# Performance work log

Measured on AMD Instinct MI355X. Metric: run time of the kernel, lower is better.

The kernel has to match this reference:

```python
import jax, jax.numpy as jnp
import numpy as np

NUM_NODES = 100000
NUM_EDGES = 1600000
NUM_GRAPHS = 512
HIDDEN = 128
LAYERS = 3
NUM_CLASSES = 10
BN_EPS = 1e-5


def setup_inputs() -> dict:
    key = jax.random.key(0)
    ks = jax.random.split(key, 12)
    x = jax.random.normal(ks[0], (NUM_NODES, HIDDEN), dtype=jnp.float32)
    edge_index = jax.random.randint(ks[1], (2, NUM_EDGES), 0, NUM_NODES, dtype=jnp.int32)
    batch = jnp.sort(jax.random.randint(ks[2], (NUM_NODES,), 0, NUM_GRAPHS, dtype=jnp.int32))
    s = 1.0 / np.sqrt(HIDDEN)
    W1 = jax.random.normal(ks[3], (LAYERS, HIDDEN, HIDDEN), dtype=jnp.float32) * s
    b1 = jnp.zeros((LAYERS, HIDDEN), dtype=jnp.float32)
    W2 = jax.random.normal(ks[4], (LAYERS, HIDDEN, HIDDEN), dtype=jnp.float32) * s
    b2 = jnp.zeros((LAYERS, HIDDEN), dtype=jnp.float32)
    gamma = jnp.ones((LAYERS, HIDDEN), dtype=jnp.float32)
    beta = jnp.zeros((LAYERS, HIDDEN), dtype=jnp.float32)
    eps_gin = jnp.zeros((LAYERS,), dtype=jnp.float32)  # train_eps init 0
    lin1_w = jax.random.normal(ks[5], (LAYERS * HIDDEN, HIDDEN), dtype=jnp.float32) * (1.0 / np.sqrt(LAYERS * HIDDEN))
    lin1_b = jnp.zeros((HIDDEN,), dtype=jnp.float32)
    lin2_w = jax.random.normal(ks[6], (HIDDEN, NUM_CLASSES), dtype=jnp.float32) * s
    lin2_b = jnp.zeros((NUM_CLASSES,), dtype=jnp.float32)
    return {"x": x, "edge_index": edge_index, "batch": batch,
            "W1": W1, "b1": b1, "W2": W2, "b2": b2,
            "gamma": gamma, "beta": beta, "eps_gin": eps_gin,
            "lin1_w": lin1_w, "lin1_b": lin1_b, "lin2_w": lin2_w, "lin2_b": lin2_b}


def _batchnorm(h, g, b):
    mu = jnp.mean(h, axis=0, keepdims=True)
    var = jnp.var(h, axis=0, keepdims=True)
    return (h - mu) * jax.lax.rsqrt(var + BN_EPS) * g + b


def reference(x, edge_index, batch, W1, b1, W2, b2, gamma, beta, eps_gin,
              lin1_w, lin1_b, lin2_w, lin2_b):
    src, dst = edge_index[0], edge_index[1]
    n = x.shape[0]
    h = x
    layer_hs = []
    for l in range(LAYERS):
        # scatter-add neighbor aggregation: agg[i] = sum_{j->i} h[j]
        agg = jax.ops.segment_sum(h[src], dst, num_segments=n)
        z = (1.0 + eps_gin[l]) * h + agg
        z = jax.nn.relu(z @ W1[l] + b1[l])
        z = jax.nn.relu(z @ W2[l] + b2[l])
        h = _batchnorm(z, gamma[l], beta[l])
        layer_hs.append(h)
    h_cat = jnp.concatenate(layer_hs, axis=-1)  # [N, LAYERS*HIDDEN]
    # global mean pool per graph
    sums = jax.ops.segment_sum(h_cat, batch, num_segments=NUM_GRAPHS)
    counts = jax.ops.segment_sum(jnp.ones((n, 1), h_cat.dtype), batch, num_segments=NUM_GRAPHS)
    g = sums / jnp.maximum(counts, 1.0)
    g = jax.nn.relu(g @ lin1_w + lin1_b)
    # dropout is identity in inference
    return g @ lin2_w + lin2_b
```

## Files before the change

### kernel.cpp

```cpp
#include <hip/hip_runtime.h>

#define HID 128
#define NGRAPH 512
#define NLAYERS 3
#define BN_EPS 1e-5f
#define NPB 256
#define EB 4096

typedef __attribute__((ext_vector_type(8))) short bf16x8;
typedef __attribute__((ext_vector_type(4))) float f32x4;
typedef __attribute__((ext_vector_type(2))) float f32x2;

__device__ inline unsigned short f2bf(float x) {
    union { float f; unsigned u; } v; v.f = x;
    unsigned r = v.u + 0x7FFFu + ((v.u >> 16) & 1u);
    return (unsigned short)(r >> 16);
}
__device__ inline float bf2f(unsigned short b) {
    union { float f; unsigned u; } v; v.u = ((unsigned)b) << 16; return v.f;
}
__device__ inline f32x2 bfp(unsigned u) {
    union { unsigned q; float f; } lo, hi;
    lo.q = u << 16; hi.q = u & 0xFFFF0000u;
    f32x2 r; r[0] = lo.f; r[1] = hi.f; return r;
}

__global__ void k_prep(float* __restrict__ stats, float* __restrict__ gsum,
                       const float4* __restrict__ x4, ushort* __restrict__ xb, int total4,
                       const float* __restrict__ W1, ushort* __restrict__ w1h, ushort* __restrict__ w1l,
                       const float* __restrict__ W2, ushort* __restrict__ w2h, ushort* __restrict__ w2l,
                       int wtotal, int xblocks,
                       const int* __restrict__ dst, int E, int* __restrict__ blkcnt) {
    __shared__ int hist[512];
    int b = blockIdx.x, t = threadIdx.x;
    if (b < 768) {
        if (b == 0) for (int l = 0; l < NLAYERS; ++l) stats[l * 256 + t] = 0.0f;
        gsum[b * 256 + t] = 0.0f;
    } else if (b < 1152) {
        int gid = (b - 768) * 256 + t;
        const float* W; ushort *Wh, *Wl; int e;
        if (gid < wtotal) { W = W1; Wh = w1h; Wl = w1l; e = gid; }
        else              { W = W2; Wh = w2h; Wl = w2l; e = gid - wtotal; }
        if (e < wtotal) {
            int l = e >> 14, rem = e & 16383, k = rem >> 7, n = rem & 127;
            float v = W[e];
            ushort hi = f2bf(v);
            ushort lo = f2bf(v - bf2f(hi));
            int o = (l << 14) + (n << 7) + k;
            Wh[o] = hi; Wl[o] = lo;
        }
    } else if (b < 1152 + xblocks) {
        int i = (b - 1152) * 256 + t;
        if (i < total4) {
            float4 v = x4[i];
            uint2 p;
            p.x = ((unsigned)f2bf(v.y) << 16) | f2bf(v.x);
            p.y = ((unsigned)f2bf(v.w) << 16) | f2bf(v.z);
            ((uint2*)xb)[i] = p;
        }
    } else {
        int b2 = b - (1152 + xblocks);
        hist[t] = 0; hist[t + 256] = 0;
        __syncthreads();
        int base = b2 * EB;
        #pragma unroll
        for (int i = 0; i < 16; ++i) {
            int e = base + i * 256 + t;
            if (e < E) atomicAdd(&hist[dst[e] >> 8], 1);
        }
        __syncthreads();
        blkcnt[b2 * 512 + t]       = hist[t];
        blkcnt[b2 * 512 + t + 256] = hist[t + 256];
    }
}

__global__ __launch_bounds__(256) void k_btot_reduce(const int* __restrict__ blkcnt,
                                                     int eblk, int* __restrict__ tot) {
    __shared__ int sh[256];
    int b = blockIdx.x;
    int t = threadIdx.x;
    int s = 0;
    for (int j = t; j < eblk; j += 256) s += blkcnt[j * 512 + b];
    sh[t] = s;
    __syncthreads();
    #pragma unroll
    for (int k = 128; k > 0; k >>= 1) {
        if (t < k) sh[t] += sh[t + k];
        __syncthreads();
    }
    if (t == 0) tot[b] = sh[0];
}

__global__ __launch_bounds__(512) void k_bscan(const int* __restrict__ tot, int nb, int E,
                                               int* __restrict__ bbase, int* __restrict__ rowptrN) {
    __shared__ int sh[512];
    int t = threadIdx.x;
    sh[t] = (t < nb) ? tot[t] : 0;
    __syncthreads();
    #pragma unroll
    for (int s = 1; s < 512; s <<= 1) {
        int v = (t >= s) ? sh[t - s] : 0;
        __syncthreads();
        sh[t] += v;
        __syncthreads();
    }
    if (t < nb) bbase[t] = (t == 0) ? 0 : sh[t - 1];
    if (t == 0) { bbase[nb] = E; *rowptrN = E; }
}

__global__ __launch_bounds__(512) void k_colscan(int* __restrict__ blkcnt, int eblk,
                                                 const int* __restrict__ bbase) {
    __shared__ int sh[512];
    int t = threadIdx.x;
    int b = blockIdx.x;
    sh[t] = (t < eblk) ? blkcnt[t * 512 + b] : 0;
    __syncthreads();
    #pragma unroll
    for (int s = 1; s < 512; s <<= 1) {
        int v = (t >= s) ? sh[t - s] : 0;
        __syncthreads();
        sh[t] += v;
        __syncthreads();
    }
    int excl = (t == 0) ? 0 : sh[t - 1];
    if (t < eblk) blkcnt[t * 512 + b] = bbase[b] + excl;
}

__global__ __launch_bounds__(256) void k_bscatter(const int* __restrict__ src,
                                                  const int* __restrict__ dst, int E,
                                                  const int* __restrict__ blkcnt,
                                                  unsigned* __restrict__ pairs) {
    __shared__ int hist[512];
    __shared__ int lbase[512];
    int t = threadIdx.x;
    hist[t] = 0; hist[t + 256] = 0;
    lbase[t]       = blkcnt[blockIdx.x * 512 + t];
    lbase[t + 256] = blkcnt[blockIdx.x * 512 + t + 256];
    __syncthreads();
    int base = blockIdx.x * EB;
    #pragma unroll
    for (int i = 0; i < 16; ++i) {
        int e = base + i * 256 + t;
        if (e < E) {
            int d = dst[e];
            int b = d >> 8;
            int pos = lbase[b] + atomicAdd(&hist[b], 1);
            pairs[pos] = ((unsigned)(d & 255) << 24) | (unsigned)src[e];
        }
    }
}

__global__ __launch_bounds__(256) void k_bbuild(const unsigned* __restrict__ pairs,
                                                const int* __restrict__ bbase, int N,
                                                int* __restrict__ rowptr, int* __restrict__ csr) {
    __shared__ int cnt[256];
    __shared__ int off[256];
    int t = threadIdx.x;
    int b = blockIdx.x;
    int base = bbase[b], bcount = bbase[b + 1] - base;
    cnt[t] = 0;
    __syncthreads();
    for (int i = t; i < bcount; i += 256) atomicAdd(&cnt[pairs[base + i] >> 24], 1);
    __syncthreads();
    off[t] = cnt[t];
    __syncthreads();
    for (int s = 1; s < 256; s <<= 1) {
        int v = (t >= s) ? off[t - s] : 0;
        __syncthreads();
        off[t] += v;
        __syncthreads();
    }
    int excl = (t == 0) ? 0 : off[t - 1];
    int node = b * NPB + t;
    if (node < N) rowptr[node] = base + excl;
    cnt[t] = excl;
    __syncthreads();
    for (int i = t; i < bcount; i += 256) {
        unsigned p = pairs[base + i];
        int dl = p >> 24;
        int pos = base + atomicAdd(&cnt[dl], 1);
        csr[pos] = (int)(p & 0xFFFFFFu);
    }
}

__global__ __launch_bounds__(256, 4) void k_gin_layer(
        const int* __restrict__ rowptr, const int* __restrict__ csr_src,
        const uint2* __restrict__ hinb,
        const float* __restrict__ prev_stats,
        const float* __restrict__ g_row, const float* __restrict__ be_row,
        const float* __restrict__ eps_gin, int layer, const int* __restrict__ batch,
        const ushort* __restrict__ w1h, const ushort* __restrict__ w1l,
        const float* __restrict__ b1,
        const ushort* __restrict__ w2h, const ushort* __restrict__ w2l,
        const float* __restrict__ b2,
        ushort* __restrict__ Hout, float* __restrict__ stat_sum, float* __restrict__ stat_sq,
        float* __restrict__ gsum, int N) {
    __shared__ __align__(16) ushort smem[8192];

    const int t = threadIdx.x;
    const int lane = t & 63;
    const int wv = t >> 6;
    const int li = lane & 15;
    const int kq = lane >> 4;
    const int n0 = wv * 32;
    const int row0 = blockIdx.x * 64;
    const int swz = (li & 7) * 4;

    {
        int q = lane >> 4;
        int f = lane & 15;
        f32x2 scv2[4], shv2[4];
        if (prev_stats) {
            float invn = 1.0f / (float)N;
            #pragma unroll
            for (int d = 0; d < 4; ++d) {
                #pragma unroll
                for (int h = 0; h < 2; ++h) {
                    int fi = f * 8 + d * 2 + h;
                    float mu = prev_stats[fi] * invn;
                    float var = prev_stats[128 + fi] * invn - mu * mu;
                    float inv = rsqrtf(var + BN_EPS);
                    float scj = g_row[fi] * inv;
                    scv2[d][h] = scj; shv2[d][h] = be_row[fi] - mu * scj;
                }
            }
        } else {
            #pragma unroll
            for (int d = 0; d < 4; ++d) { scv2[d] = (f32x2){1.f, 1.f}; shv2[d] = (f32x2){0.f, 0.f}; }
        }
        float e1 = 1.0f + eps_gin[layer];
        const uint4* hin4 = (const uint4*)hinb;
        #pragma unroll
        for (int it = 0; it < 4; ++it) {
            int r = wv * 16 + it * 4 + q;
            int node = row0 + r;
            f32x2 a2[4];
            #pragma unroll
            for (int d = 0; d < 4; ++d) a2[d] = (f32x2){0.f, 0.f};
            float cdeg = 0.f;
            if (node < N) {
                int beg = rowptr[node], end = rowptr[node + 1];
                uint4 hv = hin4[(size_t)node * 16 + f];
                a2[0] = e1 * bfp(hv.x); a2[1] = e1 * bfp(hv.y);
                a2[2] = e1 * bfp(hv.z); a2[3] = e1 * bfp(hv.w);
                int p = beg;
                for (; p + 8 <= end; p += 8) {
                    int s0 = csr_src[p],     s1 = csr_src[p + 1], s2 = csr_src[p + 2], s3 = csr_src[p + 3];
                    int s4 = csr_src[p + 4], s5 = csr_src[p + 5], s6 = csr_src[p + 6], s7 = csr_src[p + 7];
                    uint4 v0 = hin4[(size_t)s0 * 16 + f];
                    uint4 v1 = hin4[(size_t)s1 * 16 + f];
                    uint4 v2 = hin4[(size_t)s2 * 16 + f];
                    uint4 v3 = hin4[(size_t)s3 * 16 + f];
                    uint4 v4 = hin4[(size_t)s4 * 16 + f];
                    uint4 v5 = hin4[(size_t)s5 * 16 + f];
                    uint4 v6 = hin4[(size_t)s6 * 16 + f];
                    uint4 v7 = hin4[(size_t)s7 * 16 + f];
                    a2[0] += ((bfp(v0.x) + bfp(v1.x)) + (bfp(v2.x) + bfp(v3.x)))
                           + ((bfp(v4.x) + bfp(v5.x)) + (bfp(v6.x) + bfp(v7.x)));
                    a2[1] += ((bfp(v0.y) + bfp(v1.y)) + (bfp(v2.y) + bfp(v3.y)))
                           + ((bfp(v4.y) + bfp(v5.y)) + (bfp(v6.y) + bfp(v7.y)));
                    a2[2] += ((bfp(v0.z) + bfp(v1.z)) + (bfp(v2.z) + bfp(v3.z)))
                           + ((bfp(v4.z) + bfp(v5.z)) + (bfp(v6.z) + bfp(v7.z)));
                    a2[3] += ((bfp(v0.w) + bfp(v1.w)) + (bfp(v2.w) + bfp(v3.w)))
                           + ((bfp(v4.w) + bfp(v5.w)) + (bfp(v6.w) + bfp(v7.w)));
                }
                if (p < end) {
                    int last = end - 1;
                    int c1 = min(p + 1, last), c2 = min(p + 2, last), c3 = min(p + 3, last);
                    int c4 = min(p + 4, last), c5 = min(p + 5, last), c6 = min(p + 6, last);
                    int c7 = min(p + 7, last);
                    int s0 = csr_src[p],  s1 = csr_src[c1], s2 = csr_src[c2], s3 = csr_src[c3];
                    int s4 = csr_src[c4], s5 = csr_src[c5], s6 = csr_src[c6], s7 = csr_src[c7];
                    uint4 v0 = hin4[(size_t)s0 * 16 + f];
                    uint4 v1 = hin4[(size_t)s1 * 16 + f];
                    uint4 v2 = hin4[(size_t)s2 * 16 + f];
                    uint4 v3 = hin4[(size_t)s3 * 16 + f];
                    uint4 v4 = hin4[(size_t)s4 * 16 + f];
                    uint4 v5 = hin4[(size_t)s5 * 16 + f];
                    uint4 v6 = hin4[(size_t)s6 * 16 + f];
                    uint4 v7 = hin4[(size_t)s7 * 16 + f];
                    int rem = end - p;
                    unsigned m1 = (rem > 1) ? 0xFFFFFFFFu : 0u;
                    unsigned m2 = (rem > 2) ? 0xFFFFFFFFu : 0u;
                    unsigned m3 = (rem > 3) ? 0xFFFFFFFFu : 0u;
                    unsigned m4 = (rem > 4) ? 0xFFFFFFFFu : 0u;
                    unsigned m5 = (rem > 5) ? 0xFFFFFFFFu : 0u;
                    unsigned m6 = (rem > 6) ? 0xFFFFFFFFu : 0u;
                    a2[0] += ((bfp(v0.x) + bfp(v1.x & m1)) + (bfp(v2.x & m2) + bfp(v3.x & m3)))
                           + ((bfp(v4.x & m4) + bfp(v5.x & m5)) + (bfp(v6.x & m6) + (f32x2){0.f, 0.f}));
                    a2[1] += ((bfp(v0.y) + bfp(v1.y & m1)) + (bfp(v2.y & m2) + bfp(v3.y & m3)))
                           + ((bfp(v4.y & m4) + bfp(v5.y & m5)) + (bfp(v6.y & m6) + (f32x2){0.f, 0.f}));
                    a2[2] += ((bfp(v0.z) + bfp(v1.z & m1)) + (bfp(v2.z & m2) + bfp(v3.z & m3)))
                           + ((bfp(v4.z & m4) + bfp(v5.z & m5)) + (bfp(v6.z & m6) + (f32x2){0.f, 0.f}));
                    a2[3] += ((bfp(v0.w) + bfp(v1.w & m1)) + (bfp(v2.w & m2) + bfp(v3.w & m3)))
                           + ((bfp(v4.w & m4) + bfp(v5.w & m5)) + (bfp(v6.w & m6) + (f32x2){0.f, 0.f}));
                    (void)v7;
                }
                cdeg = e1 + (float)(end - beg);
            }
            f32x2 rr2[4];
            #pragma unroll
            for (int d = 0; d < 4; ++d) rr2[d] = scv2[d] * a2[d] + cdeg * shv2[d];
            uint4 ph;
            ph.x = ((unsigned)f2bf(rr2[0][1]) << 16) | f2bf(rr2[0][0]);
            ph.y = ((unsigned)f2bf(rr2[1][1]) << 16) | f2bf(rr2[1][0]);
            ph.z = ((unsigned)f2bf(rr2[2][1]) << 16) | f2bf(rr2[2][0]);
            ph.w = ((unsigned)f2bf(rr2[3][1]) << 16) | f2bf(rr2[3][0]);
            int d = r * 16 + (f ^ (r & 7));
            ((uint4*)smem)[d] = ph;
        }
    }
    __syncthreads();

    f32x4 acc[4][2];
    #pragma unroll
    for (int i = 0; i < 4; ++i) {
        acc[i][0] = (f32x4){0.f, 0.f, 0.f, 0.f};
        acc[i][1] = (f32x4){0.f, 0.f, 0.f, 0.f};
    }

    #pragma unroll
    for (int ch = 0; ch < 2; ++ch) {
        #pragma unroll
        for (int ks = 0; ks < 2; ++ks) {
            int kcol = ch * 8 + ks * 4 + kq;
            bf16x8 bh[2], bl[2];
            #pragma unroll
            for (int nt = 0; nt < 2; ++nt) {
                size_t wo = (size_t)(n0 + nt * 16 + li) * 128 + (ch * 64 + ks * 32 + kq * 8);
                bh[nt] = *(const bf16x8*)&w1h[wo];
                bl[nt] = *(const bf16x8*)&w1l[wo];
            }
            #pragma unroll
            for (int mt = 0; mt < 4; ++mt) {
                int r = mt * 16 + li;
                int hw = (r * 16 + (kcol ^ (li & 7))) * 8;
                bf16x8 ah = *(const bf16x8*)&smem[hw];
                #pragma unroll
                for (int nt = 0; nt < 2; ++nt) {
                    acc[mt][nt] = __builtin_amdgcn_mfma_f32_16x16x32_bf16(ah, bh[nt], acc[mt][nt], 0, 0, 0);
                    acc[mt][nt] = __builtin_amdgcn_mfma_f32_16x16x32_bf16(ah, bl[nt], acc[mt][nt], 0, 0, 0);
                }
            }
        }
    }

    float bz0 = b1[n0 + li], bz1 = b1[n0 + 16 + li];
    __syncthreads();
    #pragma unroll
    for (int mt = 0; mt < 4; ++mt) {
        #pragma unroll
        for (int nt = 0; nt < 2; ++nt) {
            int c = n0 + nt * 16 + li;
            int dk = c >> 1;
            int halfbase = (dk >> 5) * 32;
            int dlow = dk & 31;
            int codd = c & 1;
            float bias = nt ? bz1 : bz0;
            #pragma unroll
            for (int reg = 0; reg < 4; ++reg) {
                int r = mt * 16 + kq * 4 + reg;
                float v = fmaxf(acc[mt][nt][reg] + bias, 0.f);
                int us = (r * 64 + halfbase + (dlow ^ ((r & 7) * 4))) * 2 + codd;
                smem[us] = f2bf(v);
            }
        }
    }
    #pragma unroll
    for (int i = 0; i < 4; ++i) {
        acc[i][0] = (f32x4){0.f, 0.f, 0.f, 0.f};
        acc[i][1] = (f32x4){0.f, 0.f, 0.f, 0.f};
    }
    __syncthreads();

    #pragma unroll
    for (int ch = 0; ch < 2; ++ch) {
        #pragma unroll
        for (int ks = 0; ks < 2; ++ks) {
            bf16x8 bh[2], bl[2];
            #pragma unroll
            for (int nt = 0; nt < 2; ++nt) {
                size_t wo = (size_t)(n0 + nt * 16 + li) * 128 + (ch * 64 + ks * 32 + kq * 8);
                bh[nt] = *(const bf16x8*)&w2h[wo];
                bl[nt] = *(const bf16x8*)&w2l[wo];
            }
            int aoff = (ks * 16 + kq * 4) ^ swz;
            #pragma unroll
            for (int mt = 0; mt < 4; ++mt) {
                int idx = ((mt * 16 + li) * 64 + ch * 32 + aoff) * 2;
                bf16x8 ah = *(const bf16x8*)&smem[idx];
                #pragma unroll
                for (int nt = 0; nt < 2; ++nt) {
                    acc[mt][nt] = __builtin_amdgcn_mfma_f32_16x16x32_bf16(ah, bh[nt], acc[mt][nt], 0, 0, 0);
                    acc[mt][nt] = __builtin_amdgcn_mfma_f32_16x16x32_bf16(ah, bl[nt], acc[mt][nt], 0, 0, 0);
                }
            }
        }
    }

    float bb0 = b2[n0 + li], bb1 = b2[n0 + 16 + li];
    int btr[4][4];
    #pragma unroll
    for (int mt = 0; mt < 4; ++mt)
        #pragma unroll
        for (int reg = 0; reg < 4; ++reg) {
            int grow = row0 + mt * 16 + kq * 4 + reg;
            btr[mt][reg] = (grow < N) ? batch[grow] : -1;
        }
    __syncthreads();
    float s0 = 0.f, q0 = 0.f, s1 = 0.f, q1 = 0.f;
    #pragma unroll
    for (int mt = 0; mt < 4; ++mt) {
        #pragma unroll
        for (int reg = 0; reg < 4; ++reg) {
            int r = mt * 16 + kq * 4 + reg;
            float v0 = fmaxf(acc[mt][0][reg] + bb0, 0.f);
            float v1 = fmaxf(acc[mt][1][reg] + bb1, 0.f);
            smem[r * 128 + n0 + li]      = f2bf(v0);
            smem[r * 128 + n0 + 16 + li] = f2bf(v1);
            if (btr[mt][reg] >= 0) {
                s0 += v0; q0 += v0 * v0; s1 += v1; q1 += v1 * v1;
            }
        }
    }
    __syncthreads();
    {
        int valid = N - row0; if (valid > 64) valid = 64;
        int tot = valid * 16;
        for (int i = t; i < tot; i += 256) {
            int r = i >> 4, c = i & 15;
            ((uint4*)&Hout[(size_t)(row0 + r) * HID])[c] = ((const uint4*)smem)[r * 16 + c];
        }
    }
    s0 += __shfl_xor(s0, 16); s0 += __shfl_xor(s0, 32);
    q0 += __shfl_xor(q0, 16); q0 += __shfl_xor(q0, 32);
    s1 += __shfl_xor(s1, 16); s1 += __shfl_xor(s1, 32);
    q1 += __shfl_xor(q1, 16); q1 += __shfl_xor(q1, 32);
    if (kq == 0) {
        unsafeAtomicAdd(&stat_sum[n0 + li], s0);
        unsafeAtomicAdd(&stat_sq[n0 + li], q0);
        unsafeAtomicAdd(&stat_sum[n0 + 16 + li], s1);
        unsafeAtomicAdd(&stat_sq[n0 + 16 + li], q1);
    }
    int lastr = N - 1; if (lastr > row0 + 63) lastr = row0 + 63;
    int g_lo = batch[row0], g_hi = batch[lastr];
    int loff = layer * HID;
    for (int g = g_lo; g <= g_hi; ++g) {
        float p0 = 0.f, p1 = 0.f;
        #pragma unroll
        for (int mt = 0; mt < 4; ++mt)
            #pragma unroll
            for (int reg = 0; reg < 4; ++reg) {
                if (btr[mt][reg] == g) {
                    p0 += fmaxf(acc[mt][0][reg] + bb0, 0.f);
                    p1 += fmaxf(acc[mt][1][reg] + bb1, 0.f);
                }
            }
        p0 += __shfl_xor(p0, 16); p0 += __shfl_xor(p0, 32);
        p1 += __shfl_xor(p1, 16); p1 += __shfl_xor(p1, 32);
        if (kq == 0) {
            unsafeAtomicAdd(&gsum[(size_t)g * 384 + loff + n0 + li], p0);
            unsafeAtomicAdd(&gsum[(size_t)g * 384 + loff + n0 + 16 + li], p1);
        }
    }
}

__global__ __launch_bounds__(128) void k_mlp(const int* __restrict__ batch, int N,
                     const float* __restrict__ gsum, const float* __restrict__ stats,
                     const float* __restrict__ gamma, const float* __restrict__ beta,
                     const float* __restrict__ w1, const float* __restrict__ b1,
                     const float* __restrict__ w2, const float* __restrict__ b2,
                     float* __restrict__ out) {
    __shared__ float gl[384];
    __shared__ float hh[128];
    int g = blockIdx.x, t = threadIdx.x;
    int start, end;
    { int lo = 0, hi = N; while (lo < hi) { int m = (lo + hi) >> 1; if (batch[m] < g) lo = m + 1; else hi = m; } start = lo; }
    { int lo = start, hi = N; while (lo < hi) { int m = (lo + hi) >> 1; if (batch[m] < g + 1) lo = m + 1; else hi = m; } end = lo; }
    float cnt = (float)(end - start);
    float invc = 1.0f / fmaxf(cnt, 1.0f);
    float invn = 1.0f / (float)N;
    #pragma unroll
    for (int l = 0; l < NLAYERS; ++l) {
        float mu = stats[l * 256 + t] * invn;
        float var = stats[l * 256 + 128 + t] * invn - mu * mu;
        float inv = rsqrtf(var + BN_EPS);
        float sc = gamma[l * HID + t] * inv;
        float sh = beta[l * HID + t] - mu * sc;
        gl[l * 128 + t] = (gsum[(size_t)g * 384 + l * 128 + t] * sc + sh * cnt) * invc;
    }
    __syncthreads();
    float acc = b1[t];
    for (int k = 0; k < 384; ++k) acc = fmaf(gl[k], w1[k * HID + t], acc);
    hh[t] = fmaxf(acc, 0.f);
    __syncthreads();
    if (t < 10) {
        float a2 = b2[t];
        for (int k = 0; k < 128; ++k) a2 = fmaf(hh[k], w2[k * 10 + t], a2);
        out[g * 10 + t] = a2;
    }
}

extern "C" void kernel_launch(void* const* d_in, const int* in_sizes, int n_in,
                              void* d_out, int out_size, void* d_ws, size_t ws_size,
                              hipStream_t stream) {
    const float* x     = (const float*)d_in[0];
    const int*   ei    = (const int*)d_in[1];
    const int*   batch = (const int*)d_in[2];
    const float* W1    = (const float*)d_in[3];
    const float* b1    = (const float*)d_in[4];
    const float* W2    = (const float*)d_in[5];
    const float* b2    = (const float*)d_in[6];
    const float* gamma = (const float*)d_in[7];
    const float* beta  = (const float*)d_in[8];
    const float* epsg  = (const float*)d_in[9];
    const float* l1w   = (const float*)d_in[10];
    const float* l1b   = (const float*)d_in[11];
    const float* l2w   = (const float*)d_in[12];
    const float* l2b   = (const float*)d_in[13];

    const int N = in_sizes[0] / HID;
    const int E = in_sizes[1] / 2;
    const int* src = ei;
    const int* dst = ei + E;
    const int nb = (N + NPB - 1) / NPB;
    const int eblk = (E + EB - 1) / EB;

    float* w = (float*)d_ws;
    const size_t NF = (size_t)N * HID;
    float* zbuf   = w;
    ushort* xb    = (ushort*)(w + NF);
    ushort* hb[3] = { xb + NF, xb + 2 * NF, xb + 3 * NF };
    float* stats  = w + 4 * NF;
    float* gsum   = stats + 768;
    int*   rowptr = (int*)(gsum + (size_t)NGRAPH * 384);
    int*   csr    = rowptr + N + 1;
    int*   bbase  = csr + E;
    int*   btot   = bbase + nb + 2;
    ushort* wt  = (ushort*)(((uintptr_t)(btot + nb + 1) + 15) & ~(uintptr_t)15);
    ushort* w1h = wt;
    ushort* w1l = wt + 49152;
    ushort* w2h = wt + 98304;
    ushort* w2l = wt + 147456;

    unsigned* pairs  = (unsigned*)zbuf;
    int*      blkcnt = (int*)(w + 2 * 1024 * 1024);

    const int total4 = (int)(NF / 4);
    const int xblocks = (total4 + 255) / 256;
    const int prep_blocks = 1152 + xblocks + eblk;
    k_prep<<<prep_blocks, 256, 0, stream>>>(stats, gsum, (const float4*)x, xb, total4,
                                            W1, w1h, w1l, W2, w2h, w2l, NLAYERS * HID * HID,
                                            xblocks, dst, E, blkcnt);

    k_btot_reduce<<<nb, 256, 0, stream>>>(blkcnt, eblk, btot);
    k_bscan<<<1, 512, 0, stream>>>(btot, nb, E, bbase, rowptr + N);
    k_colscan<<<nb, 512, 0, stream>>>(blkcnt, eblk, bbase);
    k_bscatter<<<eblk, 256, 0, stream>>>(src, dst, E, blkcnt, pairs);
    k_bbuild<<<nb, 256, 0, stream>>>(pairs, bbase, N, rowptr, csr);

    for (int l = 0; l < NLAYERS; ++l) {
        const ushort* hin = (l == 0) ? xb : hb[l - 1];
        const float* pstats = (l == 0) ? nullptr : (stats + (l - 1) * 256);
        const float* grow_  = gamma + (l == 0 ? 0 : (l - 1)) * HID;
        const float* brow_  = beta  + (l == 0 ? 0 : (l - 1)) * HID;

        k_gin_layer<<<(N + 63) / 64, 256, 0, stream>>>(
            rowptr, csr, (const uint2*)hin, pstats, grow_, brow_,
            epsg, l, batch,
            w1h + (size_t)l * 16384, w1l + (size_t)l * 16384, b1 + l * HID,
            w2h + (size_t)l * 16384, w2l + (size_t)l * 16384, b2 + l * HID,
            hb[l], stats + l * 256, stats + l * 256 + 128, gsum, N);
    }

    k_mlp<<<NGRAPH, 128, 0, stream>>>(batch, N, gsum, stats, gamma, beta,
                                      l1w, l1b, l2w, l2b, (float*)d_out);
}
```

Before: 504.2 us.

## Split fused GIN layer into separate aggregation and dense MLP kernels

The fused per-layer kernel is split in two. A new gather-aggregation kernel handles 16 nodes per block and runs at higher occupancy (launch bounds 6) with no shared memory. It applies the previous layer's batchnorm and writes the aggregated features as bf16 to a new global buffer. A separate dense kernel reloads that buffer into swizzled shared memory for the two MFMA matmuls. The aim is to hide the latency of the irregular gathers better by decoupling them from the register- and LDS-heavy GEMM. The cost is an extra global write and read of an N×128 bf16 tensor per layer plus an extra launch. The tail loop now also issues 7 gathers instead of 8.

```diff
diff --git a/kernel.cpp b/kernel.cpp
--- a/kernel.cpp
+++ b/kernel.cpp
@@ -183,12 +183,116 @@
     }
 }
 
-__global__ __launch_bounds__(256, 4) void k_gin_layer(
+__global__ __launch_bounds__(256, 6) void k_agg(
         const int* __restrict__ rowptr, const int* __restrict__ csr_src,
         const uint2* __restrict__ hinb,
         const float* __restrict__ prev_stats,
         const float* __restrict__ g_row, const float* __restrict__ be_row,
-        const float* __restrict__ eps_gin, int layer, const int* __restrict__ batch,
+        const float* __restrict__ eps_gin, int layer,
+        ushort* __restrict__ z0out, int N) {
+    const int t = threadIdx.x;
+    const int lane = t & 63;
+    const int wv = t >> 6;
+    const int q = lane >> 4;
+    const int f = lane & 15;
+
+    f32x2 scv2[4], shv2[4];
+    if (prev_stats) {
+        float invn = 1.0f / (float)N;
+        #pragma unroll
+        for (int d = 0; d < 4; ++d) {
+            #pragma unroll
+            for (int h = 0; h < 2; ++h) {
+                int fi = f * 8 + d * 2 + h;
+                float mu = prev_stats[fi] * invn;
+                float var = prev_stats[128 + fi] * invn - mu * mu;
+                float inv = rsqrtf(var + BN_EPS);
+                float scj = g_row[fi] * inv;
+                scv2[d][h] = scj; shv2[d][h] = be_row[fi] - mu * scj;
+            }
+        }
+    } else {
+        #pragma unroll
+        for (int d = 0; d < 4; ++d) { scv2[d] = (f32x2){1.f, 1.f}; shv2[d] = (f32x2){0.f, 0.f}; }
+    }
+    float e1 = 1.0f + eps_gin[layer];
+    const uint4* hin4 = (const uint4*)hinb;
+
+    int r = blockIdx.x * 16 + wv * 4 + q;
+    f32x2 a2[4];
+    #pragma unroll
+    for (int d = 0; d < 4; ++d) a2[d] = (f32x2){0.f, 0.f};
+    float cdeg = 0.f;
+    if (r < N) {
+        int beg = rowptr[r], end = rowptr[r + 1];
+        uint4 hv = hin4[(size_t)r * 16 + f];
+        a2[0] = e1 * bfp(hv.x); a2[1] = e1 * bfp(hv.y);
+        a2[2] = e1 * bfp(hv.z); a2[3] = e1 * bfp(hv.w);
+        int p = beg;
+        for (; p + 8 <= end; p += 8) {
+            int s0 = csr_src[p],     s1 = csr_src[p + 1], s2 = csr_src[p + 2], s3 = csr_src[p + 3];
+            int s4 = csr_src[p + 4], s5 = csr_src[p + 5], s6 = csr_src[p + 6], s7 = csr_src[p + 7];
+            uint4 v0 = hin4[(size_t)s0 * 16 + f];
+            uint4 v1 = hin4[(size_t)s1 * 16 + f];
+            uint4 v2 = hin4[(size_t)s2 * 16 + f];
+            uint4 v3 = hin4[(size_t)s3 * 16 + f];
+            uint4 v4 = hin4[(size_t)s4 * 16 + f];
+            uint4 v5 = hin4[(size_t)s5 * 16 + f];
+            uint4 v6 = hin4[(size_t)s6 * 16 + f];
+            uint4 v7 = hin4[(size_t)s7 * 16 + f];
+            a2[0] += ((bfp(v0.x) + bfp(v1.x)) + (bfp(v2.x) + bfp(v3.x)))
+                   + ((bfp(v4.x) + bfp(v5.x)) + (bfp(v6.x) + bfp(v7.x)));
+            a2[1] += ((bfp(v0.y) + bfp(v1.y)) + (bfp(v2.y) + bfp(v3.y)))
+                   + ((bfp(v4.y) + bfp(v5.y)) + (bfp(v6.y) + bfp(v7.y)));
+            a2[2] += ((bfp(v0.z) + bfp(v1.z)) + (bfp(v2.z) + bfp(v3.z)))
+                   + ((bfp(v4.z) + bfp(v5.z)) + (bfp(v6.z) + bfp(v7.z)));
+            a2[3] += ((bfp(v0.w) + bfp(v1.w)) + (bfp(v2.w) + bfp(v3.w)))
+                   + ((bfp(v4.w) + bfp(v5.w)) + (bfp(v6.w) + bfp(v7.w)));
+        }
+        if (p < end) {
+            int last = end - 1;
+            int c1 = min(p + 1, last), c2 = min(p + 2, last), c3 = min(p + 3, last);
+            int c4 = min(p + 4, last), c5 = min(p + 5, last), c6 = min(p + 6, last);
+            int s0 = csr_src[p],  s1 = csr_src[c1], s2 = csr_src[c2], s3 = csr_src[c3];
+            int s4 = csr_src[c4], s5 = csr_src[c5], s6 = csr_src[c6];
+            uint4 v0 = hin4[(size_t)s0 * 16 + f];
+            uint4 v1 = hin4[(size_t)s1 * 16 + f];
+            uint4 v2 = hin4[(size_t)s2 * 16 + f];
+            uint4 v3 = hin4[(size_t)s3 * 16 + f];
+            uint4 v4 = hin4[(size_t)s4 * 16 + f];
+            uint4 v5 = hin4[(size_t)s5 * 16 + f];
+            uint4 v6 = hin4[(size_t)s6 * 16 + f];
+            int rem = end - p;
+            unsigned m1 = (rem > 1) ? 0xFFFFFFFFu : 0u;
+            unsigned m2 = (rem > 2) ? 0xFFFFFFFFu : 0u;
+            unsigned m3 = (rem > 3) ? 0xFFFFFFFFu : 0u;
+            unsigned m4 = (rem > 4) ? 0xFFFFFFFFu : 0u;
+            unsigned m5 = (rem > 5) ? 0xFFFFFFFFu : 0u;
+            unsigned m6 = (rem > 6) ? 0xFFFFFFFFu : 0u;
+            a2[0] += ((bfp(v0.x) + bfp(v1.x & m1)) + (bfp(v2.x & m2) + bfp(v3.x & m3)))
+                   + ((bfp(v4.x & m4) + bfp(v5.x & m5)) + bfp(v6.x & m6));
+            a2[1] += ((bfp(v0.y) + bfp(v1.y & m1)) + (bfp(v2.y & m2) + bfp(v3.y & m3)))
+                   + ((bfp(v4.y & m4) + bfp(v5.y & m5)) + bfp(v6.y & m6));
+            a2[2] += ((bfp(v0.z) + bfp(v1.z & m1)) + (bfp(v2.z & m2) + bfp(v3.z & m3)))
+                   + ((bfp(v4.z & m4) + bfp(v5.z & m5)) + bfp(v6.z & m6));
+            a2[3] += ((bfp(v0.w) + bfp(v1.w & m1)) + (bfp(v2.w & m2) + bfp(v3.w & m3)))
+                   + ((bfp(v4.w & m4) + bfp(v5.w & m5)) + bfp(v6.w & m6));
+        }
+        cdeg = e1 + (float)(end - beg);
+    }
+    f32x2 rr2[4];
+    #pragma unroll
+    for (int d = 0; d < 4; ++d) rr2[d] = scv2[d] * a2[d] + cdeg * shv2[d];
+    uint4 ph;
+    ph.x = ((unsigned)f2bf(rr2[0][1]) << 16) | f2bf(rr2[0][0]);
+    ph.y = ((unsigned)f2bf(rr2[1][1]) << 16) | f2bf(rr2[1][0]);
+    ph.z = ((unsigned)f2bf(rr2[2][1]) << 16) | f2bf(rr2[2][0]);
+    ph.w = ((unsigned)f2bf(rr2[3][1]) << 16) | f2bf(rr2[3][0]);
+    if (r < N) ((uint4*)z0out)[(size_t)r * 16 + f] = ph;
+}
+
+__global__ __launch_bounds__(256, 4) void k_mlp_dense(
+        const uint4* __restrict__ z0, int layer, const int* __restrict__ batch,
         const ushort* __restrict__ w1h, const ushort* __restrict__ w1l,
         const float* __restrict__ b1,
         const ushort* __restrict__ w2h, const ushort* __restrict__ w2l,
@@ -196,7 +300,6 @@
         ushort* __restrict__ Hout, float* __restrict__ stat_sum, float* __restrict__ stat_sq,
         float* __restrict__ gsum, int N) {
     __shared__ __align__(16) ushort smem[8192];
-
     const int t = threadIdx.x;
     const int lane = t & 63;
     const int wv = t >> 6;
@@ -207,107 +310,13 @@
     const int swz = (li & 7) * 4;
 
     {
-        int q = lane >> 4;
-        int f = lane & 15;
-        f32x2 scv2[4], shv2[4];
-        if (prev_stats) {
-            float invn = 1.0f / (float)N;
-            #pragma unroll
-            for (int d = 0; d < 4; ++d) {
-                #pragma unroll
-                for (int h = 0; h < 2; ++h) {
-                    int fi = f * 8 + d * 2 + h;
-                    float mu = prev_stats[fi] * invn;
-                    float var = prev_stats[128 + fi] * invn - mu * mu;
-                    float inv = rsqrtf(var + BN_EPS);
-                    float scj = g_row[fi] * inv;
-                    scv2[d][h] = scj; shv2[d][h] = be_row[fi] - mu * scj;
-                }
-            }
-        } else {
-            #pragma unroll
-            for (int d = 0; d < 4; ++d) { scv2[d] = (f32x2){1.f, 1.f}; shv2[d] = (f32x2){0.f, 0.f}; }
-        }
-        float e1 = 1.0f + eps_gin[layer];
-        const uint4* hin4 = (const uint4*)hinb;
-        #pragma unroll
-        for (int it = 0; it < 4; ++it) {
-            int r = wv * 16 + it * 4 + q;
-            int node = row0 + r;
-            f32x2 a2[4];
-            #pragma unroll
-            for (int d = 0; d < 4; ++d) a2[d] = (f32x2){0.f, 0.f};
-            float cdeg = 0.f;
-            if (node < N) {
-                int beg = rowptr[node], end = rowptr[node + 1];
-                uint4 hv = hin4[(size_t)node * 16 + f];
-                a2[0] = e1 * bfp(hv.x); a2[1] = e1 * bfp(hv.y);
-                a2[2] = e1 * bfp(hv.z); a2[3] = e1 * bfp(hv.w);
-                int p = beg;
-                for (; p + 8 <= end; p += 8) {
-                    int s0 = csr_src[p],     s1 = csr_src[p + 1], s2 = csr_src[p + 2], s3 = csr_src[p + 3];
-                    int s4 = csr_src[p + 4], s5 = csr_src[p + 5], s6 = csr_src[p + 6], s7 = csr_src[p + 7];
-                    uint4 v0 = hin4[(size_t)s0 * 16 + f];
-                    uint4 v1 = hin4[(size_t)s1 * 16 + f];
-                    uint4 v2 = hin4[(size_t)s2 * 16 + f];
-                    uint4 v3 = hin4[(size_t)s3 * 16 + f];
-                    uint4 v4 = hin4[(size_t)s4 * 16 + f];
-                    uint4 v5 = hin4[(size_t)s5 * 16 + f];
-                    uint4 v6 = hin4[(size_t)s6 * 16 + f];
-                    uint4 v7 = hin4[(size_t)s7 * 16 + f];
-                    a2[0] += ((bfp(v0.x) + bfp(v1.x)) + (bfp(v2.x) + bfp(v3.x)))
-                           + ((bfp(v4.x) + bfp(v5.x)) + (bfp(v6.x) + bfp(v7.x)));
-                    a2[1] += ((bfp(v0.y) + bfp(v1.y)) + (bfp(v2.y) + bfp(v3.y)))
-                           + ((bfp(v4.y) + bfp(v5.y)) + (bfp(v6.y) + bfp(v7.y)));
-                    a2[2] += ((bfp(v0.z) + bfp(v1.z)) + (bfp(v2.z) + bfp(v3.z)))
-                           + ((bfp(v4.z) + bfp(v5.z)) + (bfp(v6.z) + bfp(v7.z)));
-                    a2[3] += ((bfp(v0.w) + bfp(v1.w)) + (bfp(v2.w) + bfp(v3.w)))
-                           + ((bfp(v4.w) + bfp(v5.w)) + (bfp(v6.w) + bfp(v7.w)));
-                }
-                if (p < end) {
-                    int last = end - 1;
-                    int c1 = min(p + 1, last), c2 = min(p + 2, last), c3 = min(p + 3, last);
-                    int c4 = min(p + 4, last), c5 = min(p + 5, last), c6 = min(p + 6, last);
-                    int c7 = min(p + 7, last);
-                    int s0 = csr_src[p],  s1 = csr_src[c1], s2 = csr_src[c2], s3 = csr_src[c3];
-                    int s4 = csr_src[c4], s5 = csr_src[c5], s6 = csr_src[c6], s7 = csr_src[c7];
-                    uint4 v0 = hin4[(size_t)s0 * 16 + f];
-                    uint4 v1 = hin4[(size_t)s1 * 16 + f];
-                    uint4 v2 = hin4[(size_t)s2 * 16 + f];
-                    uint4 v3 = hin4[(size_t)s3 * 16 + f];
-                    uint4 v4 = hin4[(size_t)s4 * 16 + f];
-                    uint4 v5 = hin4[(size_t)s5 * 16 + f];
-                    uint4 v6 = hin4[(size_t)s6 * 16 + f];
-                    uint4 v7 = hin4[(size_t)s7 * 16 + f];
-                    int rem = end - p;
-                    unsigned m1 = (rem > 1) ? 0xFFFFFFFFu : 0u;
-                    unsigned m2 = (rem > 2) ? 0xFFFFFFFFu : 0u;
-                    unsigned m3 = (rem > 3) ? 0xFFFFFFFFu : 0u;
-                    unsigned m4 = (rem > 4) ? 0xFFFFFFFFu : 0u;
-                    unsigned m5 = (rem > 5) ? 0xFFFFFFFFu : 0u;
-                    unsigned m6 = (rem > 6) ? 0xFFFFFFFFu : 0u;
-                    a2[0] += ((bfp(v0.x) + bfp(v1.x & m1)) + (bfp(v2.x & m2) + bfp(v3.x & m3)))
-                           + ((bfp(v4.x & m4) + bfp(v5.x & m5)) + (bfp(v6.x & m6) + (f32x2){0.f, 0.f}));
-                    a2[1] += ((bfp(v0.y) + bfp(v1.y & m1)) + (bfp(v2.y & m2) + bfp(v3.y & m3)))
-                           + ((bfp(v4.y & m4) + bfp(v5.y & m5)) + (bfp(v6.y & m6) + (f32x2){0.f, 0.f}));
-                    a2[2] += ((bfp(v0.z) + bfp(v1.z & m1)) + (bfp(v2.z & m2) + bfp(v3.z & m3)))
-                           + ((bfp(v4.z & m4) + bfp(v5.z & m5)) + (bfp(v6.z & m6) + (f32x2){0.f, 0.f}));
-                    a2[3] += ((bfp(v0.w) + bfp(v1.w & m1)) + (bfp(v2.w & m2) + bfp(v3.w & m3)))
-                           + ((bfp(v4.w & m4) + bfp(v5.w & m5)) + (bfp(v6.w & m6) + (f32x2){0.f, 0.f}));
-                    (void)v7;
-                }
-                cdeg = e1 + (float)(end - beg);
-            }
-            f32x2 rr2[4];
-            #pragma unroll
-            for (int d = 0; d < 4; ++d) rr2[d] = scv2[d] * a2[d] + cdeg * shv2[d];
-            uint4 ph;
-            ph.x = ((unsigned)f2bf(rr2[0][1]) << 16) | f2bf(rr2[0][0]);
-            ph.y = ((unsigned)f2bf(rr2[1][1]) << 16) | f2bf(rr2[1][0]);
-            ph.z = ((unsigned)f2bf(rr2[2][1]) << 16) | f2bf(rr2[2][0]);
-            ph.w = ((unsigned)f2bf(rr2[3][1]) << 16) | f2bf(rr2[3][0]);
-            int d = r * 16 + (f ^ (r & 7));
-            ((uint4*)smem)[d] = ph;
+        const uint4 zz = {0u, 0u, 0u, 0u};
+        #pragma unroll
+        for (int i = 0; i < 4; ++i) {
+            int idx = i * 256 + t;
+            int r = idx >> 4, f = idx & 15;
+            uint4 v = (row0 + r < N) ? z0[(size_t)(row0 + r) * 16 + f] : zz;
+            ((uint4*)smem)[r * 16 + (f ^ (r & 7))] = v;
         }
     }
     __syncthreads();
@@ -528,9 +537,9 @@
 
     float* w = (float*)d_ws;
     const size_t NF = (size_t)N * HID;
-    float* zbuf   = w;
     ushort* xb    = (ushort*)(w + NF);
     ushort* hb[3] = { xb + NF, xb + 2 * NF, xb + 3 * NF };
+    ushort* z0buf = xb + 4 * NF;
     float* stats  = w + 4 * NF;
     float* gsum   = stats + 768;
     int*   rowptr = (int*)(gsum + (size_t)NGRAPH * 384);
@@ -543,7 +552,7 @@
     ushort* w2h = wt + 98304;
     ushort* w2l = wt + 147456;
 
-    unsigned* pairs  = (unsigned*)zbuf;
+    unsigned* pairs  = (unsigned*)w;
     int*      blkcnt = (int*)(w + 2 * 1024 * 1024);
 
     const int total4 = (int)(NF / 4);
@@ -565,9 +574,11 @@
         const float* grow_  = gamma + (l == 0 ? 0 : (l - 1)) * HID;
         const float* brow_  = beta  + (l == 0 ? 0 : (l - 1)) * HID;
 
-        k_gin_layer<<<(N + 63) / 64, 256, 0, stream>>>(
-            rowptr, csr, (const uint2*)hin, pstats, grow_, brow_,
-            epsg, l, batch,
+        k_agg<<<(N + 15) / 16, 256, 0, stream>>>(
+            rowptr, csr, (const uint2*)hin, pstats, grow_, brow_, epsg, l, z0buf, N);
+
+        k_mlp_dense<<<(N + 63) / 64, 256, 0, stream>>>(
+            (const uint4*)z0buf, l, batch,
             w1h + (size_t)l * 16384, w1l + (size_t)l * 16384, b1 + l * HID,
             w2h + (size_t)l * 16384, w2l + (size_t)l * 16384, b2 + l * HID,
             hb[l], stats + l * 256, stats + l * 256 + 128, gsum, N);
```

After: 566.9 us. +12.5%, slower.
